# Kernel tuning notes

Hardware: AMD Instinct MI355X
Metric: run time of the kernel (lower is better)

Reference implementation:

```python
import jax, jax.numpy as jnp
import numpy as np

K = 16  # centroids per codebook (4-bit LUT indices, blink-mm convention)


def _im2col(x, kh, kw, stride, pad):
    # x: [B, C, H, W] -> [B, P, C*kh*kw] with channel-major feature ordering
    # (each length-(kh*kw) subvector is one channel's patch, matching the
    #  per-channel codebook layout of the 3x3 AMM conv).
    B, C, H, W = x.shape
    xp = jnp.pad(x, ((0, 0), (0, 0), (pad, pad), (pad, pad)))
    Ho = (H + 2 * pad - kh) // stride + 1
    Wo = (W + 2 * pad - kw) // stride + 1
    cols = [xp[:, :, i:i + stride * Ho:stride, j:j + stride * Wo:stride]
            for i in range(kh) for j in range(kw)]  # fixed small loop (<=9)
    feat = jnp.stack(cols, axis=2)                      # [B, C, kh*kw, Ho, Wo]
    feat = feat.reshape(B, C * kh * kw, Ho, Wo)
    feat = feat.transpose(0, 2, 3, 1).reshape(B, Ho * Wo, C * kh * kw)
    return feat, Ho, Wo


def _amm_conv_bn_act(x, centroids, lut, scale, bias, kernel, stride, pad, relu):
    # Product-quantization approximate matmul conv:
    #  1) im2col, split feature dim D into ncodebooks subspaces of dim dsub
    #  2) nearest-centroid (L2) assignment per subspace -> 4-bit index
    #  3) gather+accumulate precomputed LUT dot products over codebooks
    #  4) folded BatchNorm affine + optional ReLU
    feat, Ho, Wo = _im2col(x, kernel, kernel, stride, pad)
    B, P, D = feat.shape
    ncb, k, dsub = centroids.shape
    xs = feat.reshape(B, P, ncb, dsub)
    dots = jnp.einsum('bpcd,ckd->bpck', xs, centroids)          # [B,P,ncb,K]
    c2 = jnp.sum(centroids * centroids, axis=-1)                # [ncb,K]
    idx = jnp.argmin(c2[None, None] - 2.0 * dots, axis=-1)      # [B,P,ncb]
    onehot = jax.nn.one_hot(idx, k, dtype=x.dtype)              # [B,P,ncb,K]
    out = jnp.einsum('bpck,cko->bpo', onehot, lut)              # LUT accumulate
    out = out * scale + bias                                    # folded BN
    if relu:
        out = jax.nn.relu(out)
    Cout = lut.shape[-1]
    return out.reshape(B, Ho, Wo, Cout).transpose(0, 3, 1, 2)


def setup_inputs() -> dict:
    key = jax.random.key(0)
    ks = jax.random.split(key, 16)
    inplanes, planes, width = 1024, 256, 256
    B, H, W = 32, 14, 14
    d = {}
    d['x'] = jax.random.normal(ks[0], (B, inplanes, H, W), dtype=jnp.float32)
    d['c1_centroids'] = jax.random.normal(ks[1], (inplanes // 4, K, 4), dtype=jnp.float32)
    d['c1_lut'] = jax.random.normal(ks[2], (inplanes // 4, K, width), dtype=jnp.float32) * 0.1
    d['c1_scale'] = jax.random.uniform(ks[3], (width,), dtype=jnp.float32, minval=0.5, maxval=1.5)
    d['c1_bias'] = jax.random.normal(ks[4], (width,), dtype=jnp.float32) * 0.1
    d['c2_centroids'] = jax.random.normal(ks[5], (width, K, 9), dtype=jnp.float32)
    d['c2_lut'] = jax.random.normal(ks[6], (width, K, width), dtype=jnp.float32) * 0.1
    d['c2_scale'] = jax.random.uniform(ks[7], (width,), dtype=jnp.float32, minval=0.5, maxval=1.5)
    d['c2_bias'] = jax.random.normal(ks[8], (width,), dtype=jnp.float32) * 0.1
    d['c3_centroids'] = jax.random.normal(ks[9], (width // 4, K, 4), dtype=jnp.float32)
    d['c3_lut'] = jax.random.normal(ks[10], (width // 4, K, planes * 4), dtype=jnp.float32) * 0.1
    d['c3_scale'] = jax.random.uniform(ks[11], (planes * 4,), dtype=jnp.float32, minval=0.5, maxval=1.5)
    d['c3_bias'] = jax.random.normal(ks[12], (planes * 4,), dtype=jnp.float32) * 0.1
    return d


def reference(x, c1_centroids, c1_lut, c1_scale, c1_bias,
              c2_centroids, c2_lut, c2_scale, c2_bias,
              c3_centroids, c3_lut, c3_scale, c3_bias):
    identity = x
    out = _amm_conv_bn_act(x, c1_centroids, c1_lut, c1_scale, c1_bias,
                           kernel=1, stride=1, pad=0, relu=True)
    out = _amm_conv_bn_act(out, c2_centroids, c2_lut, c2_scale, c2_bias,
                           kernel=3, stride=1, pad=1, relu=True)
    out = _amm_conv_bn_act(out, c3_centroids, c3_lut, c3_scale, c3_bias,
                           kernel=1, stride=1, pad=0, relu=False)
    # QuantizedAdd + QuantizedReLU (float reference math: add then relu)
    return jax.nn.relu(out + identity)
```

## Files before the change

kernel.cpp:

```cpp
#include <hip/hip_runtime.h>
#include <stdint.h>

#define PP 196
#define BP 6272

typedef _Float16 half_t;
typedef half_t half8v __attribute__((ext_vector_type(8)));
typedef half_t half4v __attribute__((ext_vector_type(4)));
typedef half_t half2v __attribute__((ext_vector_type(2)));


template <typename T>
__global__ __launch_bounds__(256) void assign_1x1(
    const T* __restrict__ in, const float* __restrict__ cents,
    uint32_t* __restrict__ idxp, int nchan) {
  __shared__ float  sf[8][16][4];
  __shared__ double sd[8][16][6];
  const int chunk = blockIdx.y;
  const int t = threadIdx.x;
  for (int i = t; i < 512; i += 256) {
    float c = cents[(size_t)chunk * 512 + i];
    int cb = i >> 6, r = i & 63;
    sf[cb][r >> 2][r & 3] = c;
    sd[cb][r >> 2][1 + (r & 3)] = (double)c;
  }
  __syncthreads();
  if (t < 128) {
    int cb = t >> 4, k = t & 15;
    double s = 0.0;
#pragma unroll
    for (int d = 0; d < 4; d++) { double c = sd[cb][k][1 + d]; s += c * c; }
    sd[cb][k][0] = s;
  }
  __syncthreads();
  const int p = blockIdx.x * 256 + t;
  if (p >= BP) return;
  const unsigned b = (unsigned)p / 196u;
  const unsigned pr = (unsigned)p - b * 196u;
  const T* xb = in + ((size_t)b * nchan + chunk * 32) * PP + pr;
  T xr[32];
#pragma unroll
  for (int i = 0; i < 32; i++) xr[i] = xb[(size_t)i * PP];
  float xs2[32];
#pragma unroll
  for (int i = 0; i < 32; i++) xs2[i] = 2.f * (float)xr[i];
  uint32_t word = 0;
#pragma unroll 1
  for (int cb = 0; cb < 8; cb++) {
    float best = 1e30f, sec = 1e30f; int bi = 0;
#pragma unroll
    for (int k = 0; k < 16; k++) {
      const float4 c = *(const float4*)&sf[cb][k][0];
      float dist = c.x * (c.x - xs2[cb * 4 + 0]);
      dist = fmaf(c.y, c.y - xs2[cb * 4 + 1], dist);
      dist = fmaf(c.z, c.z - xs2[cb * 4 + 2], dist);
      dist = fmaf(c.w, c.w - xs2[cb * 4 + 3], dist);
      if (dist < best) { sec = best; best = dist; bi = k; }
      else sec = fminf(sec, dist);
    }
    if (__any(sec - best < 2e-4f)) {
      double xv[4];
#pragma unroll
      for (int d = 0; d < 4; d++) xv[d] = (double)xr[cb * 4 + d];
      double bb = 1e300; int bi64 = 0;
#pragma unroll
      for (int k = 0; k < 16; k++) {
        double dot = 0.0;
#pragma unroll
        for (int d = 0; d < 4; d++) dot = fma(xv[d], sd[cb][k][1 + d], dot);
        double dist = sd[cb][k][0] - 2.0 * dot;
        if (dist < bb) { bb = dist; bi64 = k; }
      }
      bi = bi64;
    }
    word |= (uint32_t)bi << (4 * cb);
  }
  idxp[(size_t)chunk * BP + p] = word;
}

__global__ __launch_bounds__(256) void assign_3x3(
    const double* __restrict__ in, const float* __restrict__ cents,
    uint32_t* __restrict__ idxp) {
  __shared__ float  sf[8][16][12];
  __shared__ double sd[8][16][10];
  const int chunk = blockIdx.y;
  const int c0g = chunk * 8;
  const int t = threadIdx.x;
  for (int i = t; i < 1152; i += 256) {
    int cb = i / 144, r = i - cb * 144;
    int k = r / 9, d = r - k * 9;
    float c = cents[(size_t)(c0g + cb) * 144 + k * 9 + d];
    sf[cb][k][1 + d] = c;
    sd[cb][k][1 + d] = (double)c;
  }
  __syncthreads();
  if (t < 128) {
    int cb = t >> 4, k = t & 15;
    double s = 0.0;
    float s32 = 0.f;
#pragma unroll
    for (int d = 0; d < 9; d++) {
      double c = sd[cb][k][1 + d]; s += c * c;
      float cf = sf[cb][k][1 + d]; s32 += cf * cf;
    }
    sd[cb][k][0] = s;
    sf[cb][k][0] = s32;
  }
  __syncthreads();
  const int p = blockIdx.x * 256 + t;
  if (p >= BP) return;
  const unsigned b = (unsigned)p / 196u;
  const unsigned pr = (unsigned)p - b * 196u;
  const int oh = pr / 14, ow = pr - oh * 14;
  uint32_t word = 0;
#pragma unroll 1
  for (int cb = 0; cb < 8; cb++) {
    const double* base = in + ((size_t)b * 256 + (c0g + cb)) * PP;
    double v64[9]; float v32[9];
#pragma unroll
    for (int r = 0; r < 3; r++) {
#pragma unroll
      for (int cc = 0; cc < 3; cc++) {
        int hh = oh + r - 1, ww = ow + cc - 1;
        bool ok = (hh >= 0) & (hh < 14) & (ww >= 0) & (ww < 14);
        double v = ok ? base[hh * 14 + ww] : 0.0;
        v64[r * 3 + cc] = v;
        v32[r * 3 + cc] = (float)v;
      }
    }
    float best = 1e30f, sec = 1e30f; int bi = 0;
#pragma unroll
    for (int k = 0; k < 16; k++) {
      const float4 cA = *(const float4*)&sf[cb][k][0];
      const float4 cB = *(const float4*)&sf[cb][k][4];
      const float4 cC = *(const float4*)&sf[cb][k][8];
      float dot = v32[0] * cA.y;
      dot = fmaf(v32[1], cA.z, dot);
      dot = fmaf(v32[2], cA.w, dot);
      dot = fmaf(v32[3], cB.x, dot);
      dot = fmaf(v32[4], cB.y, dot);
      dot = fmaf(v32[5], cB.z, dot);
      dot = fmaf(v32[6], cB.w, dot);
      dot = fmaf(v32[7], cC.x, dot);
      dot = fmaf(v32[8], cC.y, dot);
      float dist = fmaf(-2.f, dot, cA.x);
      if (dist < best) { sec = best; best = dist; bi = k; }
      else sec = fminf(sec, dist);
    }
    if (__any(sec - best < 4e-4f)) {
      double bb = 1e300; int bi64 = 0;
#pragma unroll
      for (int k = 0; k < 16; k++) {
        double dot = 0.0;
#pragma unroll
        for (int d = 0; d < 9; d++) dot = fma(v64[d], sd[cb][k][1 + d], dot);
        double dist = sd[cb][k][0] - 2.0 * dot;
        if (dist < bb) { bb = dist; bi64 = k; }
      }
      bi = bi64;
    }
    word |= (uint32_t)bi << (4 * cb);
  }
  idxp[(size_t)chunk * BP + p] = word;
}

template <int NCB, int NOUT, bool RELU, bool FUSE3, typename OutT>
__global__ __launch_bounds__(256) void accum_f64(
    const float* __restrict__ lut, const uint32_t* __restrict__ idxp,
    const float* __restrict__ scale, const float* __restrict__ bias,
    const float* __restrict__ c3cent, uint8_t* __restrict__ i3b,
    OutT* __restrict__ out) {
  __shared__ float s_lut[4096];
  __shared__ float  c3f[4][16][4];
  __shared__ float  c3c2f[4][16];
  __shared__ double c3d[4][16][4];
  __shared__ double c3c2d[4][16];
  const int t = threadIdx.x;
  const int lane = t & 63;
  const int q = t >> 6;
  const int p = blockIdx.x * 64 + lane;
  const int o_base = blockIdx.y * 16;
  if (FUSE3 && t < 64) {
    int cb_l = t >> 4, k = t & 15;
    const float4 cf = *(const float4*)(c3cent + ((size_t)(blockIdx.y * 4 + cb_l)) * 64 + k * 4);
    c3f[cb_l][k][0] = cf.x; c3f[cb_l][k][1] = cf.y;
    c3f[cb_l][k][2] = cf.z; c3f[cb_l][k][3] = cf.w;
    double d0 = (double)cf.x, d1 = (double)cf.y, d2 = (double)cf.z, d3 = (double)cf.w;
    c3d[cb_l][k][0] = d0; c3d[cb_l][k][1] = d1;
    c3d[cb_l][k][2] = d2; c3d[cb_l][k][3] = d3;
    double s = 0.0; s += d0 * d0; s += d1 * d1; s += d2 * d2; s += d3 * d3;
    c3c2d[cb_l][k] = s;
    float s32 = 0.f; s32 += cf.x * cf.x; s32 += cf.y * cf.y;
    s32 += cf.z * cf.z; s32 += cf.w * cf.w;
    c3c2f[cb_l][k] = s32;
  }
  const float* src = lut + ((size_t)(t >> 6) * 16 + ((t >> 2) & 15)) * NOUT
                         + o_base + (t & 3) * 4;
  const int kk = (t >> 2) & 15, qs = t & 3;
  const int sslot = (t >> 6) * 64 + qs * 16 + (kk ^ (2 * qs));
  const int q2 = q * 2;
  double a0 = 0, a1 = 0, a2 = 0, a3 = 0;
  constexpr int NCHUNK = NCB / 16;
  for (int ch = 0; ch < NCHUNK; ch++) {
    __syncthreads();
    uint32_t w0 = idxp[(size_t)(ch * 2) * BP + p];
    uint32_t w1 = idxp[(size_t)(ch * 2 + 1) * BP + p];
    {
      const float* g = src + (size_t)(ch * 256) * NOUT;
#pragma unroll
      for (int j = 0; j < 4; j++) {
        float4 v = *(const float4*)(g + (size_t)(64 * j) * NOUT);
        *(float4*)(s_lut + (sslot + 256 * j) * 4) = v;
      }
    }
    __syncthreads();
    const float* buf = s_lut + q * 64;
#pragma unroll
    for (int jq = 0; jq < 4; jq++) {
      uint32_t w = (jq < 2) ? w0 : w1;
      int sh = (jq & 1) * 16;
      int i0 = (int)((w >> sh) & 15u);
      int i1 = (int)((w >> (sh + 4)) & 15u);
      int i2 = (int)((w >> (sh + 8)) & 15u);
      int i3 = (int)((w >> (sh + 12)) & 15u);
      const float4 va = *(const float4*)(buf + (4 * jq)     * 256 + (i0 ^ q2) * 4);
      const float4 vb = *(const float4*)(buf + (4 * jq + 1) * 256 + (i1 ^ q2) * 4);
      const float4 vc = *(const float4*)(buf + (4 * jq + 2) * 256 + (i2 ^ q2) * 4);
      const float4 vd = *(const float4*)(buf + (4 * jq + 3) * 256 + (i3 ^ q2) * 4);
      float s0 = (va.x + vb.x) + (vc.x + vd.x);
      float s1 = (va.y + vb.y) + (vc.y + vd.y);
      float s2 = (va.z + vb.z) + (vc.z + vd.z);
      float s3 = (va.w + vb.w) + (vc.w + vd.w);
      a0 += (double)s0; a1 += (double)s1; a2 += (double)s2; a3 += (double)s3;
    }
  }
  const unsigned b = (unsigned)p / 196u;
  const unsigned pr = (unsigned)p - b * 196u;
  const int o = o_base + q * 4;
  const float4 sc = *(const float4*)(scale + o);
  const float4 bs = *(const float4*)(bias + o);
  double r0 = a0 * (double)sc.x + (double)bs.x;
  double r1 = a1 * (double)sc.y + (double)bs.y;
  double r2 = a2 * (double)sc.z + (double)bs.z;
  double r3 = a3 * (double)sc.w + (double)bs.w;
  if (RELU) {
    r0 = fmax(r0, 0.0); r1 = fmax(r1, 0.0);
    r2 = fmax(r2, 0.0); r3 = fmax(r3, 0.0);
  }
  if (FUSE3) {
    const int cb_l = q;
    float x0 = (float)r0, x1 = (float)r1, x2 = (float)r2, x3 = (float)r3;
    float best = 1e30f, sec = 1e30f; int bi = 0;
#pragma unroll
    for (int k = 0; k < 16; k++) {
      const float4 c = *(const float4*)&c3f[cb_l][k][0];
      float dot = x0 * c.x;
      dot = fmaf(x1, c.y, dot);
      dot = fmaf(x2, c.z, dot);
      dot = fmaf(x3, c.w, dot);
      float dist = fmaf(-2.f, dot, c3c2f[cb_l][k]);
      if (dist < best) { sec = best; best = dist; bi = k; }
      else sec = fminf(sec, dist);
    }
    if (__any(sec - best < 1e-3f)) {
      double bb = 1e300; int bi64 = 0;
#pragma unroll
      for (int k = 0; k < 16; k++) {
        double dot = 0.0;
        dot = fma(r0, c3d[cb_l][k][0], dot);
        dot = fma(r1, c3d[cb_l][k][1], dot);
        dot = fma(r2, c3d[cb_l][k][2], dot);
        dot = fma(r3, c3d[cb_l][k][3], dot);
        double dist = c3c2d[cb_l][k] - 2.0 * dot;
        if (dist < bb) { bb = dist; bi64 = k; }
      }
      bi = bi64;
    }
    i3b[((size_t)(blockIdx.y >> 2) * BP + p) * 16 + (blockIdx.y & 3) * 4 + q] =
        (uint8_t)bi;
  } else {
    OutT* op = out + ((size_t)b * NOUT + o) * PP + pr;
    op[0 * PP] = (OutT)r0; op[1 * PP] = (OutT)r1;
    op[2 * PP] = (OutT)r2; op[3 * PP] = (OutT)r3;
  }
}

__global__ __launch_bounds__(256) void accum3_f16(
    const float* __restrict__ lut, const uint8_t* __restrict__ i3b,
    const float* __restrict__ scale, const float* __restrict__ bias,
    const float* __restrict__ res, float* __restrict__ out) {
  __shared__ half_t s16[16 * 640];
  const int t = threadIdx.x;
  const int lane = t & 63;
  const int wave = t >> 6;
  const int h = wave & 1;
  const int pg = wave >> 1;
  const int p = blockIdx.x * 128 + pg * 64 + lane;
  const int o_base = blockIdx.y * 16;
  const int rs = t >> 2, cg = t & 3;
  const size_t cs = (size_t)16 * 16 * 1024;
  constexpr int NCHUNK = 4;
  float acc[8];
#pragma unroll
  for (int i = 0; i < 8; i++) acc[i] = 0.f;
  for (int ch = 0; ch < NCHUNK; ch++) {
    __syncthreads();
    const uint4 iw = *(const uint4*)(i3b + ((size_t)ch * BP + p) * 16);
    {
#pragma unroll
      for (int j = 0; j < 4; j++) {
        const int r = rs + 64 * j;
        const float4 v = *(const float4*)(lut + (size_t)ch * cs +
                                          (size_t)r * 1024 + o_base + cg * 4);
        half4v hv;
        hv[0] = (half_t)v.x; hv[1] = (half_t)v.y;
        hv[2] = (half_t)v.z; hv[3] = (half_t)v.w;
        *(half4v*)(s16 + (r >> 4) * 640 + (r & 15) * 40 + cg * 4) = hv;
      }
    }
    __syncthreads();
#pragma unroll
    for (int grp = 0; grp < 2; grp++) {
      uint32_t wa = grp ? iw.z : iw.x;
      uint32_t wb = grp ? iw.w : iw.y;
      half2v p0 = 0, p1 = 0, p2 = 0, p3 = 0;
#pragma unroll
      for (int j = 0; j < 8; j++) {
        uint32_t w = (j < 4) ? wa : wb;
        int idx = (int)((w >> ((j & 3) * 8)) & 15u);
        int cb_l = grp * 8 + j;
        const half8v v = *(const half8v*)(s16 + cb_l * 640 + idx * 40 + h * 8);
        const half2v* vp = (const half2v*)&v;
        p0 += vp[0]; p1 += vp[1]; p2 += vp[2]; p3 += vp[3];
      }
      acc[0] += (float)p0[0]; acc[1] += (float)p0[1];
      acc[2] += (float)p1[0]; acc[3] += (float)p1[1];
      acc[4] += (float)p2[0]; acc[5] += (float)p2[1];
      acc[6] += (float)p3[0]; acc[7] += (float)p3[1];
    }
  }
  const unsigned b = (unsigned)p / 196u;
  const unsigned pr = (unsigned)p - b * 196u;
  const int o = o_base + h * 8;
  const float* rp = res + ((size_t)b * 1024 + o) * PP + pr;
  float* op = out + ((size_t)b * 1024 + o) * PP + pr;
#pragma unroll
  for (int i = 0; i < 8; i++) {
    float v = acc[i] * scale[o + i] + bias[o + i] + rp[(size_t)i * PP];
    op[(size_t)i * PP] = fmaxf(v, 0.f);
  }
}


extern "C" void kernel_launch(void* const* d_in, const int* in_sizes, int n_in,
                              void* d_out, int out_size, void* d_ws, size_t ws_size,
                              hipStream_t stream) {
  const float* x   = (const float*)d_in[0];
  const float* c1c = (const float*)d_in[1];
  const float* c1l = (const float*)d_in[2];
  const float* c1s = (const float*)d_in[3];
  const float* c1b = (const float*)d_in[4];
  const float* c2c = (const float*)d_in[5];
  const float* c2l = (const float*)d_in[6];
  const float* c2s = (const float*)d_in[7];
  const float* c2b = (const float*)d_in[8];
  const float* c3c = (const float*)d_in[9];
  const float* c3l = (const float*)d_in[10];
  const float* c3s = (const float*)d_in[11];
  const float* c3b = (const float*)d_in[12];

  const size_t sz_i1  = (size_t)32 * BP * 4;
  const size_t sz_i2  = (size_t)32 * BP * 4;
  const size_t sz_i3b = (size_t)BP * 64;
  const size_t sz_o64 = (size_t)BP * 256 * 8;

  char* w = (char*)d_ws;
  uint32_t* i1 = (uint32_t*)w; w += sz_i1;
  uint32_t* i2 = (uint32_t*)w; w += sz_i2;
  uint8_t* i3b = (uint8_t*)w;  w += sz_i3b;
  double* out1;
  if (ws_size >= (size_t)(w - (char*)d_ws) + sz_o64) {
    out1 = (double*)w;
  } else {
    out1 = (double*)d_out;
  }

  const dim3 blkA(256), blkC(256);
  assign_1x1<float><<<dim3(25, 32), blkA, 0, stream>>>(x, c1c, i1, 1024);
  accum_f64<256, 256, true, false, double><<<dim3(98, 16), blkC, 0, stream>>>(
      c1l, i1, c1s, c1b, nullptr, nullptr, out1);
  assign_3x3<<<dim3(25, 32), blkA, 0, stream>>>(out1, c2c, i2);
  accum_f64<256, 256, true, true, double><<<dim3(98, 16), blkC, 0, stream>>>(
      c2l, i2, c2s, c2b, c3c, i3b, nullptr);
  accum3_f16<<<dim3(49, 64), blkC, 0, stream>>>(
      c3l, i3b, c3s, c3b, x, (float*)d_out);
}
```

Measured before the change: 226.7 us.

## Process two pixels per thread in LUT accumulate and add fp32 activation copy for 3x3 assign

The LUT-accumulate kernel now handles two 64-pixel groups per block, so each shared-memory LUT tile staged from global memory serves twice as many pixels and the grid halves. The first accumulate also writes an fp32 copy of its activations, which lets the 3x3 assignment kernel read 4-byte values on the common path and fetch the double copy only when the fp32 margin test triggers the fallback. In exchange, the first accumulate kernel writes an extra buffer, uses more registers, and the fallback path can land in d_out if the workspace is too small.

```diff
diff --git a/kernel.cpp b/kernel.cpp
--- a/kernel.cpp
+++ b/kernel.cpp
@@ -79,8 +79,8 @@
 }
 
 __global__ __launch_bounds__(256) void assign_3x3(
-    const double* __restrict__ in, const float* __restrict__ cents,
-    uint32_t* __restrict__ idxp) {
+    const double* __restrict__ in, const float* __restrict__ inf,
+    const float* __restrict__ cents, uint32_t* __restrict__ idxp) {
   __shared__ float  sf[8][16][12];
   __shared__ double sd[8][16][10];
   const int chunk = blockIdx.y;
@@ -112,22 +112,23 @@
   const unsigned b = (unsigned)p / 196u;
   const unsigned pr = (unsigned)p - b * 196u;
   const int oh = pr / 14, ow = pr - oh * 14;
+  int  noff[9]; bool nok[9];
+#pragma unroll
+  for (int r = 0; r < 3; r++) {
+#pragma unroll
+    for (int cc = 0; cc < 3; cc++) {
+      int hh = oh + r - 1, ww = ow + cc - 1;
+      nok[r * 3 + cc] = (hh >= 0) & (hh < 14) & (ww >= 0) & (ww < 14);
+      noff[r * 3 + cc] = hh * 14 + ww;
+    }
+  }
   uint32_t word = 0;
 #pragma unroll 1
   for (int cb = 0; cb < 8; cb++) {
-    const double* base = in + ((size_t)b * 256 + (c0g + cb)) * PP;
-    double v64[9]; float v32[9];
-#pragma unroll
-    for (int r = 0; r < 3; r++) {
-#pragma unroll
-      for (int cc = 0; cc < 3; cc++) {
-        int hh = oh + r - 1, ww = ow + cc - 1;
-        bool ok = (hh >= 0) & (hh < 14) & (ww >= 0) & (ww < 14);
-        double v = ok ? base[hh * 14 + ww] : 0.0;
-        v64[r * 3 + cc] = v;
-        v32[r * 3 + cc] = (float)v;
-      }
-    }
+    const float* basef = inf + ((size_t)b * 256 + (c0g + cb)) * PP;
+    float v32[9];
+#pragma unroll
+    for (int i = 0; i < 9; i++) v32[i] = nok[i] ? basef[noff[i]] : 0.f;
     float best = 1e30f, sec = 1e30f; int bi = 0;
 #pragma unroll
     for (int k = 0; k < 16; k++) {
@@ -148,6 +149,10 @@
       else sec = fminf(sec, dist);
     }
     if (__any(sec - best < 4e-4f)) {
+      const double* base = in + ((size_t)b * 256 + (c0g + cb)) * PP;
+      double v64[9];
+#pragma unroll
+      for (int i = 0; i < 9; i++) v64[i] = nok[i] ? base[noff[i]] : 0.0;
       double bb = 1e300; int bi64 = 0;
 #pragma unroll
       for (int k = 0; k < 16; k++) {
@@ -169,7 +174,7 @@
     const float* __restrict__ lut, const uint32_t* __restrict__ idxp,
     const float* __restrict__ scale, const float* __restrict__ bias,
     const float* __restrict__ c3cent, uint8_t* __restrict__ i3b,
-    OutT* __restrict__ out) {
+    OutT* __restrict__ out, float* __restrict__ outf) {
   __shared__ float s_lut[4096];
   __shared__ float  c3f[4][16][4];
   __shared__ float  c3c2f[4][16];
@@ -178,7 +183,8 @@
   const int t = threadIdx.x;
   const int lane = t & 63;
   const int q = t >> 6;
-  const int p = blockIdx.x * 64 + lane;
+  const int p0 = blockIdx.x * 128 + lane;
+  const int p1 = p0 + 64;
   const int o_base = blockIdx.y * 16;
   if (FUSE3 && t < 64) {
     int cb_l = t >> 4, k = t & 15;
@@ -199,12 +205,15 @@
   const int kk = (t >> 2) & 15, qs = t & 3;
   const int sslot = (t >> 6) * 64 + qs * 16 + (kk ^ (2 * qs));
   const int q2 = q * 2;
-  double a0 = 0, a1 = 0, a2 = 0, a3 = 0;
+  double aA0 = 0, aA1 = 0, aA2 = 0, aA3 = 0;
+  double aB0 = 0, aB1 = 0, aB2 = 0, aB3 = 0;
   constexpr int NCHUNK = NCB / 16;
   for (int ch = 0; ch < NCHUNK; ch++) {
     __syncthreads();
-    uint32_t w0 = idxp[(size_t)(ch * 2) * BP + p];
-    uint32_t w1 = idxp[(size_t)(ch * 2 + 1) * BP + p];
+    uint32_t wA0 = idxp[(size_t)(ch * 2) * BP + p0];
+    uint32_t wA1 = idxp[(size_t)(ch * 2 + 1) * BP + p0];
+    uint32_t wB0 = idxp[(size_t)(ch * 2) * BP + p1];
+    uint32_t wB1 = idxp[(size_t)(ch * 2 + 1) * BP + p1];
     {
       const float* g = src + (size_t)(ch * 256) * NOUT;
 #pragma unroll
@@ -217,71 +226,103 @@
     const float* buf = s_lut + q * 64;
 #pragma unroll
     for (int jq = 0; jq < 4; jq++) {
-      uint32_t w = (jq < 2) ? w0 : w1;
+      const int cbb = 4 * jq * 256;
+      uint32_t ua = (jq < 2) ? wA0 : wA1;
+      uint32_t ub = (jq < 2) ? wB0 : wB1;
       int sh = (jq & 1) * 16;
-      int i0 = (int)((w >> sh) & 15u);
-      int i1 = (int)((w >> (sh + 4)) & 15u);
-      int i2 = (int)((w >> (sh + 8)) & 15u);
-      int i3 = (int)((w >> (sh + 12)) & 15u);
-      const float4 va = *(const float4*)(buf + (4 * jq)     * 256 + (i0 ^ q2) * 4);
-      const float4 vb = *(const float4*)(buf + (4 * jq + 1) * 256 + (i1 ^ q2) * 4);
-      const float4 vc = *(const float4*)(buf + (4 * jq + 2) * 256 + (i2 ^ q2) * 4);
-      const float4 vd = *(const float4*)(buf + (4 * jq + 3) * 256 + (i3 ^ q2) * 4);
-      float s0 = (va.x + vb.x) + (vc.x + vd.x);
-      float s1 = (va.y + vb.y) + (vc.y + vd.y);
-      float s2 = (va.z + vb.z) + (vc.z + vd.z);
-      float s3 = (va.w + vb.w) + (vc.w + vd.w);
-      a0 += (double)s0; a1 += (double)s1; a2 += (double)s2; a3 += (double)s3;
-    }
-  }
-  const unsigned b = (unsigned)p / 196u;
-  const unsigned pr = (unsigned)p - b * 196u;
+      {
+        int i0 = (int)((ua >> sh) & 15u);
+        int i1 = (int)((ua >> (sh + 4)) & 15u);
+        int i2 = (int)((ua >> (sh + 8)) & 15u);
+        int i3 = (int)((ua >> (sh + 12)) & 15u);
+        const float4 va = *(const float4*)(buf + cbb       + (i0 ^ q2) * 4);
+        const float4 vb = *(const float4*)(buf + cbb + 256 + (i1 ^ q2) * 4);
+        const float4 vc = *(const float4*)(buf + cbb + 512 + (i2 ^ q2) * 4);
+        const float4 vd = *(const float4*)(buf + cbb + 768 + (i3 ^ q2) * 4);
+        float s0 = (va.x + vb.x) + (vc.x + vd.x);
+        float s1 = (va.y + vb.y) + (vc.y + vd.y);
+        float s2 = (va.z + vb.z) + (vc.z + vd.z);
+        float s3 = (va.w + vb.w) + (vc.w + vd.w);
+        aA0 += (double)s0; aA1 += (double)s1; aA2 += (double)s2; aA3 += (double)s3;
+      }
+      {
+        int i0 = (int)((ub >> sh) & 15u);
+        int i1 = (int)((ub >> (sh + 4)) & 15u);
+        int i2 = (int)((ub >> (sh + 8)) & 15u);
+        int i3 = (int)((ub >> (sh + 12)) & 15u);
+        const float4 va = *(const float4*)(buf + cbb       + (i0 ^ q2) * 4);
+        const float4 vb = *(const float4*)(buf + cbb + 256 + (i1 ^ q2) * 4);
+        const float4 vc = *(const float4*)(buf + cbb + 512 + (i2 ^ q2) * 4);
+        const float4 vd = *(const float4*)(buf + cbb + 768 + (i3 ^ q2) * 4);
+        float s0 = (va.x + vb.x) + (vc.x + vd.x);
+        float s1 = (va.y + vb.y) + (vc.y + vd.y);
+        float s2 = (va.z + vb.z) + (vc.z + vd.z);
+        float s3 = (va.w + vb.w) + (vc.w + vd.w);
+        aB0 += (double)s0; aB1 += (double)s1; aB2 += (double)s2; aB3 += (double)s3;
+      }
+    }
+  }
   const int o = o_base + q * 4;
   const float4 sc = *(const float4*)(scale + o);
   const float4 bs = *(const float4*)(bias + o);
-  double r0 = a0 * (double)sc.x + (double)bs.x;
-  double r1 = a1 * (double)sc.y + (double)bs.y;
-  double r2 = a2 * (double)sc.z + (double)bs.z;
-  double r3 = a3 * (double)sc.w + (double)bs.w;
-  if (RELU) {
-    r0 = fmax(r0, 0.0); r1 = fmax(r1, 0.0);
-    r2 = fmax(r2, 0.0); r3 = fmax(r3, 0.0);
-  }
-  if (FUSE3) {
-    const int cb_l = q;
-    float x0 = (float)r0, x1 = (float)r1, x2 = (float)r2, x3 = (float)r3;
-    float best = 1e30f, sec = 1e30f; int bi = 0;
-#pragma unroll
-    for (int k = 0; k < 16; k++) {
-      const float4 c = *(const float4*)&c3f[cb_l][k][0];
-      float dot = x0 * c.x;
-      dot = fmaf(x1, c.y, dot);
-      dot = fmaf(x2, c.z, dot);
-      dot = fmaf(x3, c.w, dot);
-      float dist = fmaf(-2.f, dot, c3c2f[cb_l][k]);
-      if (dist < best) { sec = best; best = dist; bi = k; }
-      else sec = fminf(sec, dist);
-    }
-    if (__any(sec - best < 1e-3f)) {
-      double bb = 1e300; int bi64 = 0;
+#pragma unroll
+  for (int pi = 0; pi < 2; pi++) {
+    const int p = pi ? p1 : p0;
+    double a0 = pi ? aB0 : aA0;
+    double a1 = pi ? aB1 : aA1;
+    double a2 = pi ? aB2 : aA2;
+    double a3 = pi ? aB3 : aA3;
+    const unsigned b = (unsigned)p / 196u;
+    const unsigned pr = (unsigned)p - b * 196u;
+    double r0 = a0 * (double)sc.x + (double)bs.x;
+    double r1 = a1 * (double)sc.y + (double)bs.y;
+    double r2 = a2 * (double)sc.z + (double)bs.z;
+    double r3 = a3 * (double)sc.w + (double)bs.w;
+    if (RELU) {
+      r0 = fmax(r0, 0.0); r1 = fmax(r1, 0.0);
+      r2 = fmax(r2, 0.0); r3 = fmax(r3, 0.0);
+    }
+    if (FUSE3) {
+      const int cb_l = q;
+      float x0 = (float)r0, x1 = (float)r1, x2 = (float)r2, x3 = (float)r3;
+      float best = 1e30f, sec = 1e30f; int bi = 0;
 #pragma unroll
       for (int k = 0; k < 16; k++) {
-        double dot = 0.0;
-        dot = fma(r0, c3d[cb_l][k][0], dot);
-        dot = fma(r1, c3d[cb_l][k][1], dot);
-        dot = fma(r2, c3d[cb_l][k][2], dot);
-        dot = fma(r3, c3d[cb_l][k][3], dot);
-        double dist = c3c2d[cb_l][k] - 2.0 * dot;
-        if (dist < bb) { bb = dist; bi64 = k; }
-      }
-      bi = bi64;
-    }
-    i3b[((size_t)(blockIdx.y >> 2) * BP + p) * 16 + (blockIdx.y & 3) * 4 + q] =
-        (uint8_t)bi;
-  } else {
-    OutT* op = out + ((size_t)b * NOUT + o) * PP + pr;
-    op[0 * PP] = (OutT)r0; op[1 * PP] = (OutT)r1;
-    op[2 * PP] = (OutT)r2; op[3 * PP] = (OutT)r3;
+        const float4 c = *(const float4*)&c3f[cb_l][k][0];
+        float dot = x0 * c.x;
+        dot = fmaf(x1, c.y, dot);
+        dot = fmaf(x2, c.z, dot);
+        dot = fmaf(x3, c.w, dot);
+        float dist = fmaf(-2.f, dot, c3c2f[cb_l][k]);
+        if (dist < best) { sec = best; best = dist; bi = k; }
+        else sec = fminf(sec, dist);
+      }
+      if (__any(sec - best < 1e-3f)) {
+        double bb = 1e300; int bi64 = 0;
+#pragma unroll
+        for (int k = 0; k < 16; k++) {
+          double dot = 0.0;
+          dot = fma(r0, c3d[cb_l][k][0], dot);
+          dot = fma(r1, c3d[cb_l][k][1], dot);
+          dot = fma(r2, c3d[cb_l][k][2], dot);
+          dot = fma(r3, c3d[cb_l][k][3], dot);
+          double dist = c3c2d[cb_l][k] - 2.0 * dot;
+          if (dist < bb) { bb = dist; bi64 = k; }
+        }
+        bi = bi64;
+      }
+      i3b[((size_t)(blockIdx.y >> 2) * BP + p) * 16 + (blockIdx.y & 3) * 4 + q] =
+          (uint8_t)bi;
+    } else {
+      OutT* op = out + ((size_t)b * NOUT + o) * PP + pr;
+      op[0 * PP] = (OutT)r0; op[1 * PP] = (OutT)r1;
+      op[2 * PP] = (OutT)r2; op[3 * PP] = (OutT)r3;
+      if (outf) {
+        float* ofp = outf + ((size_t)b * NOUT + o) * PP + pr;
+        ofp[0 * PP] = (float)r0; ofp[1 * PP] = (float)r1;
+        ofp[2 * PP] = (float)r2; ofp[3 * PP] = (float)r3;
+      }
+    }
   }
 }
 
@@ -373,25 +414,29 @@
   const size_t sz_i2  = (size_t)32 * BP * 4;
   const size_t sz_i3b = (size_t)BP * 64;
   const size_t sz_o64 = (size_t)BP * 256 * 8;
+  const size_t sz_o32 = (size_t)BP * 256 * 4;
 
   char* w = (char*)d_ws;
   uint32_t* i1 = (uint32_t*)w; w += sz_i1;
   uint32_t* i2 = (uint32_t*)w; w += sz_i2;
   uint8_t* i3b = (uint8_t*)w;  w += sz_i3b;
   double* out1;
-  if (ws_size >= (size_t)(w - (char*)d_ws) + sz_o64) {
-    out1 = (double*)w;
+  float* out1f;
+  if (ws_size >= (size_t)(w - (char*)d_ws) + sz_o64 + sz_o32) {
+    out1 = (double*)w; w += sz_o64;
+    out1f = (float*)w;
   } else {
     out1 = (double*)d_out;
+    out1f = (float*)((char*)d_out + sz_o64);
   }
 
   const dim3 blkA(256), blkC(256);
   assign_1x1<float><<<dim3(25, 32), blkA, 0, stream>>>(x, c1c, i1, 1024);
-  accum_f64<256, 256, true, false, double><<<dim3(98, 16), blkC, 0, stream>>>(
-      c1l, i1, c1s, c1b, nullptr, nullptr, out1);
-  assign_3x3<<<dim3(25, 32), blkA, 0, stream>>>(out1, c2c, i2);
-  accum_f64<256, 256, true, true, double><<<dim3(98, 16), blkC, 0, stream>>>(
-      c2l, i2, c2s, c2b, c3c, i3b, nullptr);
+  accum_f64<256, 256, true, false, double><<<dim3(49, 16), blkC, 0, stream>>>(
+      c1l, i1, c1s, c1b, nullptr, nullptr, out1, out1f);
+  assign_3x3<<<dim3(25, 32), blkA, 0, stream>>>(out1, out1f, c2c, i2);
+  accum_f64<256, 256, true, true, double><<<dim3(49, 16), blkC, 0, stream>>>(
+      c2l, i2, c2s, c2b, c3c, i3b, nullptr, nullptr);
   accum3_f16<<<dim3(49, 64), blkC, 0, stream>>>(
       c3l, i3b, c3s, c3b, x, (float*)d_out);
 }
```

Measured after the change: 234.9 us. +3.6%, slower.
